# Kernel tuning notes

Hardware: AMD Instinct MI355X
Metric: run time of the kernel (lower is better)

The kernel has to match this reference:

```python
import jax, jax.numpy as jnp
import numpy as np

EMB = 1024
HEAD = 64
RANK = 8
LRA_SCL = 2.0
LORA = 1.0


def setup_inputs() -> dict:
    key = jax.random.key(0)
    ks = jax.random.split(key, 12)
    s = 1.0 / np.sqrt(EMB)
    sr = 1.0 / np.sqrt(RANK)
    inp = {
        "batEmb": jax.random.normal(ks[0], (8, 2048, EMB), dtype=jnp.float32),
        "tokMrk": jax.random.randint(ks[1], (8, 2048), 0, 2, dtype=jnp.int32),
        # base projections, nn.Linear weight layout [out, in]
        "Wq": jax.random.uniform(ks[2], (HEAD, EMB), jnp.float32, -s, s),
        "Wk": jax.random.uniform(ks[3], (HEAD, EMB), jnp.float32, -s, s),
        "Wv": jax.random.uniform(ks[4], (HEAD, EMB), jnp.float32, -s, s),
        # LoRA: A [rank, emb], B [head, rank]. (Original inits B to zero; we
        # randomize with small scale so the LoRA path is numerically exercised.)
        "Aq": jax.random.uniform(ks[5], (RANK, EMB), jnp.float32, -s, s),
        "Bq": jax.random.uniform(ks[6], (HEAD, RANK), jnp.float32, -sr, sr) * 0.02,
        "Ak": jax.random.uniform(ks[7], (RANK, EMB), jnp.float32, -s, s),
        "Bk": jax.random.uniform(ks[8], (HEAD, RANK), jnp.float32, -sr, sr) * 0.02,
        "Av": jax.random.uniform(ks[9], (RANK, EMB), jnp.float32, -s, s),
        "Bv": jax.random.uniform(ks[10], (HEAD, RANK), jnp.float32, -sr, sr) * 0.02,
    }
    return inp


def _proj(x, W, A, B):
    # base + LoRA low-rank delta (dropout = identity in eval)
    base = jnp.einsum('bse,he->bsh', x, W)
    lora = jnp.einsum('bsr,hr->bsh', jnp.einsum('bse,re->bsr', x, A), B)
    return base + lora * (LRA_SCL * LORA)


def reference(batEmb, tokMrk, Wq, Wk, Wv, Aq, Bq, Ak, Bk, Av, Bv):
    q = _proj(batEmb, Wq, Aq, Bq)  # [B,S,H]
    k = _proj(batEmb, Wk, Ak, Bk)
    v = _proj(batEmb, Wv, Av, Bv)
    w = jnp.einsum('bqh,bkh->bqk', q, k) * (HEAD ** -0.5)  # [B,S,S]
    mask = (tokMrk == 0)[:, None, :]  # [B,1,S] over key dim
    w = jnp.where(mask, -jnp.inf, w)
    w = jax.nn.softmax(w, axis=-1)
    w = jnp.nan_to_num(w, nan=0.0)
    return jnp.einsum('bqk,bkh->bqh', w, v)
```

## Files before the change

### kernel.cpp

```cpp
#include <hip/hip_runtime.h>
#include <hip/hip_bf16.h>
#include <stdint.h>

#define EMB 1024
#define NB 8
#define SEQ 2048
#define RANK 8
#define SPLIT 4

#define BM 64
#define BK 64
#define NSTG 16
#define BUFB 40960
#define NBUF 3

typedef __attribute__((ext_vector_type(8))) short bf16x8;
typedef __attribute__((ext_vector_type(4))) float f32x4;
typedef unsigned short u16;
typedef unsigned int u32;

__device__ __forceinline__ u16 f2bf(float f) {
  u32 u = __builtin_bit_cast(u32, f);
  u = (u + 0x7fffu + ((u >> 16) & 1u)) >> 16;
  return (u16)u;
}
__device__ __forceinline__ u32 pk2(float lo, float hi) {
  return (u32)f2bf(lo) | ((u32)f2bf(hi) << 16);
}
__device__ __forceinline__ u32 cvtpk(float lo, float hi) {
  __hip_bfloat162 h = __float22bfloat162_rn(make_float2(lo, hi));
  u32 u; __builtin_memcpy(&u, &h, 4); return u;
}
__device__ __forceinline__ void gll16(const void* g, void* l) {
  __builtin_amdgcn_global_load_lds(
      (const __attribute__((address_space(1))) unsigned int*)g,
      (__attribute__((address_space(3))) unsigned int*)l, 16, 0, 0);
}

#define PBAR()   asm volatile("s_barrier" ::: "memory")
#define WAITV(n) asm volatile("s_waitcnt vmcnt(" #n ")" ::: "memory")

__global__ __launch_bounds__(256) void fold_k(
    const float* __restrict__ Wq, const float* __restrict__ Wk, const float* __restrict__ Wv,
    const float* __restrict__ Aq, const float* __restrict__ Bq,
    const float* __restrict__ Ak, const float* __restrict__ Bk,
    const float* __restrict__ Av, const float* __restrict__ Bv,
    u16* __restrict__ weff) {
  int m = blockIdx.x;
  int mat = m >> 6, h = m & 63;
  const float* W = mat == 0 ? Wq : (mat == 1 ? Wk : Wv);
  const float* A = mat == 0 ? Aq : (mat == 1 ? Ak : Av);
  const float* B = mat == 0 ? Bq : (mat == 1 ? Bk : Bv);
  float bb[RANK];
#pragma unroll
  for (int r = 0; r < RANK; r++) bb[r] = 2.0f * B[h * RANK + r];
  int e = threadIdx.x * 4;
  float4 w4 = *(const float4*)(W + h * EMB + e);
  float a0 = w4.x, a1 = w4.y, a2 = w4.z, a3 = w4.w;
#pragma unroll
  for (int r = 0; r < RANK; r++) {
    float4 av = *(const float4*)(A + r * EMB + e);
    a0 += bb[r] * av.x; a1 += bb[r] * av.y; a2 += bb[r] * av.z; a3 += bb[r] * av.w;
  }
  u16* o = weff + (size_t)m * EMB + e;
  o[0] = f2bf(a0); o[1] = f2bf(a1); o[2] = f2bf(a2); o[3] = f2bf(a3);
}

__global__ __launch_bounds__(320) void proj_k(
    const float* __restrict__ X, const u16* __restrict__ weff,
    u16* __restrict__ qws, u16* __restrict__ kws, u16* __restrict__ vws) {
  extern __shared__ __align__(16) char smem[];

  int t = threadIdx.x;
  int w = t >> 6, l = t & 63;
  int rbase = blockIdx.x * BM;

  if (w >= 3) {
    int q = w - 3;
    int wkoff = ((l & 7) ^ (l >> 3)) * 8;
    int wc0 = l >> 3;
    int lr4 = l >> 4;
    int l15 = l & 15;

#define ISSUE(st, bufp) do {                                                   \
    _Pragma("unroll")                                                          \
    for (int i_ = 0; i_ < 8; i_++) {                                           \
      int rrel_ = q * 32 + i_ * 4 + lr4;                                       \
      int xo_ = 4 * (l15 ^ (rrel_ & 7));        \
      gll16(X + (size_t)(rbase + rrel_) * EMB + (st) * BK + xo_,               \
            (bufp) + q * 8192 + i_ * 1024);                                    \
    }                                                                          \
    _Pragma("unroll")                                                          \
    for (int i_ = 0; i_ < 12; i_++) { int wj_ = q * 12 + i_;                   \
      gll16(weff + (size_t)(wj_ * 8 + wc0) * EMB + (st) * BK + wkoff,          \
            (bufp) + 16384 + wj_ * 1024);                                      \
    } } while (0)

    ISSUE(0, smem);
    ISSUE(1, smem + BUFB);
    WAITV(20);
    for (int s = 0; s < NSTG; s++) {
      PBAR();
      if (s + 2 < NSTG) {
        ISSUE(s + 2, smem + ((s + 2) % NBUF) * BUFB);
        WAITV(20);
      } else if (s + 1 < NSTG) {
        WAITV(0);
      }
    }
#undef ISSUE
  } else {
    int l15 = l & 15, lh = l >> 4;
    f32x4 acc[4][4];
    f32x4 zero = {0.f, 0.f, 0.f, 0.f};
#pragma unroll
    for (int rt = 0; rt < 4; rt++)
#pragma unroll
      for (int ct = 0; ct < 4; ct++) acc[rt][ct] = zero;

    for (int s = 0; s < NSTG; s++) {
      PBAR();
      const char* bx = smem + (s % NBUF) * BUFB;
      const char* bw = bx + 16384;
#pragma unroll
      for (int j = 0; j < 2; j++) {
        bf16x8 a[4];
#pragma unroll
        for (int rt = 0; rt < 4; rt++) {
          int r = rt * 16 + l15;
          int sw = (r & 7) << 4;
          const char* base = bx + r * 256;
          f32x4 lo = *(const f32x4*)(base + ((j * 128 + lh * 32) ^ sw));
          f32x4 hi = *(const f32x4*)(base + ((j * 128 + lh * 32 + 16) ^ sw));
          union { bf16x8 v; u32 u[4]; } au;
          au.u[0] = cvtpk(lo.x, lo.y); au.u[1] = cvtpk(lo.z, lo.w);
          au.u[2] = cvtpk(hi.x, hi.y); au.u[3] = cvtpk(hi.z, hi.w);
          a[rt] = au.v;
        }
        __builtin_amdgcn_s_setprio(1);
#pragma unroll
        for (int ct = 0; ct < 4; ct++) {
          int col = w * 64 + ct * 16 + l15;
          bf16x8 bf = *(const bf16x8*)(bw + col * 128 +
                                       ((j * 64 + lh * 16) ^ ((col & 7) << 4)));
#pragma unroll
          for (int rt = 0; rt < 4; rt++)
            acc[rt][ct] = __builtin_amdgcn_mfma_f32_16x16x32_bf16(a[rt], bf, acc[rt][ct], 0, 0, 0);
        }
        __builtin_amdgcn_s_setprio(0);
      }
    }

#pragma unroll
    for (int rt = 0; rt < 4; rt++)
#pragma unroll
      for (int ct = 0; ct < 4; ct++) {
        int c = w * 64 + ct * 16 + l15;
#pragma unroll
        for (int r = 0; r < 4; r++) {
          int rr = rbase + rt * 16 + lh * 4 + r;
          float av = acc[rt][ct][r];
          if (c < 64) av *= 0.125f;
          u16 v = f2bf(av);
          if (c < 64) {
            qws[(size_t)rr * 64 + c] = v;
          } else if (c < 128) {
            kws[(size_t)rr * 64 + (c - 64)] = v;
          } else {
            int bb = rr >> 11, tok = rr & 2047;
            vws[((size_t)(bb * 64 + (c - 128))) * SEQ + tok] = v;
          }
        }
      }
  }
}

__global__ __launch_bounds__(256) void attn_k(
    const u16* __restrict__ qws, const u16* __restrict__ kws, const u16* __restrict__ vws,
    const int* __restrict__ mrk,
    float* __restrict__ po, float* __restrict__ pmp, float* __restrict__ plp) {
  __shared__ __align__(16) u16 ks[2 * 4096];
  __shared__ __align__(16) u16 vt[2 * 4096];
  __shared__ __align__(16) u16 ps[4 * 1024];

  int b = blockIdx.y;
  int z = blockIdx.z;
  int q0 = blockIdx.x * 64;
  int t = threadIdx.x;
  int w = t >> 6, l = t & 63;
  int l15 = l & 15, lh = l >> 4;

  int srow = t >> 3;
  int ssw = (((t & 7) << 4) ^ ((srow & 7) << 4)) >> 1;
  char* ksb = (char*)ks + w * 1024;
  char* vtb = (char*)vt + w * 1024;

  const u16* qp = qws + ((size_t)(b * SEQ + q0 + w * 16 + l15)) * 64 + lh * 8;
  bf16x8 qb0 = *(const bf16x8*)qp;
  bf16x8 qb1 = *(const bf16x8*)(qp + 32);

  f32x4 o[4];
  f32x4 zero = {0.f, 0.f, 0.f, 0.f};
#pragma unroll
  for (int ht = 0; ht < 4; ht++) o[ht] = zero;
  float mrow = -30000.0f, lrow = 0.f;

  int swz = (l15 & 7) << 4;
  int koffA = ((lh << 4) ^ swz) >> 1;
  int koffB = ((64 | (lh << 4)) ^ swz) >> 1;
  u16* psw = ps + w * 1024 + l15 * 64;

  const int NC = SEQ / 64 / SPLIT;
  int kk0 = z * (SEQ / SPLIT);

#define STAGE_KV(buf, kk)                                                          \
  do {                                                                             \
    gll16(kws + ((size_t)(b * SEQ + (kk) + srow)) * 64 + ssw,                      \
          ksb + (buf) * 8192);                                                     \
    gll16(kws + ((size_t)(b * SEQ + (kk) + srow + 32)) * 64 + ssw,                 \
          ksb + (buf) * 8192 + 4096);                                              \
    gll16(vws + ((size_t)(b * 64 + srow)) * SEQ + (kk) + ssw,                      \
          vtb + (buf) * 8192);                                                     \
    gll16(vws + ((size_t)(b * 64 + srow + 32)) * SEQ + (kk) + ssw,                 \
          vtb + (buf) * 8192 + 4096);                                              \
  } while (0)

  STAGE_KV(0, kk0);
  __syncthreads();

  int cur = 0;
  for (int kc = 0; kc < NC; kc++) {
    int kk = kk0 + kc * 64;
    if (kc + 1 < NC) STAGE_KV(cur ^ 1, kk + 64);

    int4 mi[4];
#pragma unroll
    for (int nt = 0; nt < 4; nt++)
      mi[nt] = *(const int4*)(mrk + b * SEQ + kk + nt * 16 + lh * 4);

    const u16* kb = ks + cur * 4096;
    f32x4 sa[4];
    __builtin_amdgcn_s_setprio(1);
#pragma unroll
    for (int nt = 0; nt < 4; nt++) {
      const u16* kr = kb + (nt * 16 + l15) * 64;
      bf16x8 k0 = *(const bf16x8*)(kr + koffA);
      bf16x8 k1 = *(const bf16x8*)(kr + koffB);
      f32x4 s = zero;
      s = __builtin_amdgcn_mfma_f32_16x16x32_bf16(k0, qb0, s, 0, 0, 0);
      s = __builtin_amdgcn_mfma_f32_16x16x32_bf16(k1, qb1, s, 0, 0, 0);
      sa[nt] = s;
    }
    __builtin_amdgcn_s_setprio(0);

    const u16* vbb = vt + cur * 4096;
    bf16x8 vb[4][2];
#pragma unroll
    for (int ht = 0; ht < 4; ht++) {
      const u16* vr = vbb + (ht * 16 + l15) * 64;
      vb[ht][0] = *(const bf16x8*)(vr + koffA);
      vb[ht][1] = *(const bf16x8*)(vr + koffB);
    }

#pragma unroll
    for (int nt = 0; nt < 4; nt++) {
      sa[nt][0] = mi[nt].x ? sa[nt][0] : -INFINITY;
      sa[nt][1] = mi[nt].y ? sa[nt][1] : -INFINITY;
      sa[nt][2] = mi[nt].z ? sa[nt][2] : -INFINITY;
      sa[nt][3] = mi[nt].w ? sa[nt][3] : -INFINITY;
    }
    float t0 = fmaxf(fmaxf(sa[0][0], sa[0][1]), fmaxf(sa[0][2], sa[0][3]));
    float t1 = fmaxf(fmaxf(sa[1][0], sa[1][1]), fmaxf(sa[1][2], sa[1][3]));
    float t2 = fmaxf(fmaxf(sa[2][0], sa[2][1]), fmaxf(sa[2][2], sa[2][3]));
    float t3 = fmaxf(fmaxf(sa[3][0], sa[3][1]), fmaxf(sa[3][2], sa[3][3]));
    float tm = fmaxf(fmaxf(t0, t1), fmaxf(t2, t3));
    tm = fmaxf(tm, __shfl_xor(tm, 16));
    tm = fmaxf(tm, __shfl_xor(tm, 32));

    if (!__all(tm <= mrow + 8.0f)) {
      float nm = fmaxf(mrow, tm);
      float alpha = __expf(mrow - nm);
      mrow = nm;
      lrow *= alpha;
      float a0 = __shfl(alpha, lh * 4 + 0);
      float a1 = __shfl(alpha, lh * 4 + 1);
      float a2 = __shfl(alpha, lh * 4 + 2);
      float a3 = __shfl(alpha, lh * 4 + 3);
#pragma unroll
      for (int ht = 0; ht < 4; ht++) {
        o[ht][0] *= a0; o[ht][1] *= a1; o[ht][2] *= a2; o[ht][3] *= a3;
      }
    }

    float ts = 0.f;
#pragma unroll
    for (int nt = 0; nt < 4; nt++) {
#pragma unroll
      for (int r = 0; r < 4; r++) {
        float p = __expf(sa[nt][r] - mrow);
        sa[nt][r] = p;
        ts += p;
      }
    }
    ts += __shfl_xor(ts, 16);
    ts += __shfl_xor(ts, 32);
    lrow += ts;

#pragma unroll
    for (int nt = 0; nt < 4; nt++) {
      u32 plo = pk2(sa[nt][0], sa[nt][1]);
      u32 phi = pk2(sa[nt][2], sa[nt][3]);
      *(uint2*)&psw[(((nt * 32 + lh * 8) ^ swz) >> 1)] = make_uint2(plo, phi);
    }
    bf16x8 ap0 = *(const bf16x8*)(psw + koffA);
    bf16x8 ap1 = *(const bf16x8*)(psw + koffB);

    __builtin_amdgcn_s_setprio(1);
#pragma unroll
    for (int ht = 0; ht < 4; ht++) {
      o[ht] = __builtin_amdgcn_mfma_f32_16x16x32_bf16(ap0, vb[ht][0], o[ht], 0, 0, 0);
      o[ht] = __builtin_amdgcn_mfma_f32_16x16x32_bf16(ap1, vb[ht][1], o[ht], 0, 0, 0);
    }
    __builtin_amdgcn_s_setprio(0);
    __syncthreads();
    cur ^= 1;
  }
#undef STAGE_KV

#pragma unroll
  for (int r = 0; r < 4; r++) {
    int rr = q0 + w * 16 + lh * 4 + r;
    float* pob = po + ((size_t)z * NB * SEQ + (size_t)b * SEQ + rr) * 64;
#pragma unroll
    for (int ht = 0; ht < 4; ht++) pob[ht * 16 + l15] = o[ht][r];
  }
  if (lh == 0) {
    int rr = q0 + w * 16 + l15;
    pmp[(size_t)z * NB * SEQ + (size_t)b * SEQ + rr] = mrow;
    plp[(size_t)z * NB * SEQ + (size_t)b * SEQ + rr] = lrow;
  }
}

__global__ __launch_bounds__(256) void merge_k(
    const float* __restrict__ po, const float* __restrict__ pmp,
    const float* __restrict__ plp, float* __restrict__ out) {
  int tid = threadIdx.x;
  int row = blockIdx.x * 32 + (tid >> 3);
  int c8 = (tid & 7) * 8;
  const int RT = NB * SEQ;

  float m[SPLIT], lv[SPLIT];
  float M = -INFINITY;
#pragma unroll
  for (int s = 0; s < SPLIT; s++) {
    m[s] = pmp[(size_t)s * RT + row];
    lv[s] = plp[(size_t)s * RT + row];
    M = fmaxf(M, m[s]);
  }
  float o8[8];
#pragma unroll
  for (int j = 0; j < 8; j++) o8[j] = 0.f;
  float L = 0.f;
  if (M != -INFINITY) {
#pragma unroll
    for (int s = 0; s < SPLIT; s++) {
      float ws = __expf(m[s] - M);
      L += ws * lv[s];
      const float* p = po + ((size_t)s * RT + row) * 64 + c8;
#pragma unroll
      for (int j = 0; j < 8; j++) o8[j] += ws * p[j];
    }
  }
  float inv = (L > 0.f) ? 1.0f / L : 0.f;
  float* op = out + (size_t)row * 64 + c8;
#pragma unroll
  for (int j = 0; j < 8; j++) op[j] = o8[j] * inv;
}

extern "C" void kernel_launch(void* const* d_in, const int* in_sizes, int n_in,
                              void* d_out, int out_size, void* d_ws, size_t ws_size,
                              hipStream_t stream) {
  const float* X   = (const float*)d_in[0];
  const int*   mrk = (const int*)d_in[1];
  const float* Wq  = (const float*)d_in[2];
  const float* Wk  = (const float*)d_in[3];
  const float* Wv  = (const float*)d_in[4];
  const float* Aq  = (const float*)d_in[5];
  const float* Bq  = (const float*)d_in[6];
  const float* Ak  = (const float*)d_in[7];
  const float* Bk  = (const float*)d_in[8];
  const float* Av  = (const float*)d_in[9];
  const float* Bv  = (const float*)d_in[10];

  u16* weff = (u16*)d_ws;
  u16* qws  = (u16*)((char*)d_ws + (512 << 10));
  u16* kws  = qws + (size_t)16384 * 64;
  u16* vws  = kws + (size_t)16384 * 64;
  float* po  = (float*)((char*)d_ws + ((size_t)6656 << 10));
  float* pmp = po + (size_t)SPLIT * 16384 * 64;
  float* plp = pmp + (size_t)SPLIT * 16384;

  (void)hipFuncSetAttribute((const void*)proj_k,
                            hipFuncAttributeMaxDynamicSharedMemorySize, NBUF * BUFB);

  fold_k<<<192, 256, 0, stream>>>(Wq, Wk, Wv, Aq, Bq, Ak, Bk, Av, Bv, weff);
  proj_k<<<256, 320, NBUF * BUFB, stream>>>(X, weff, qws, kws, vws);
  attn_k<<<dim3(32, 8, SPLIT), 256, 0, stream>>>(qws, kws, vws, mrk, po, pmp, plp);
  merge_k<<<512, 256, 0, stream>>>(po, pmp, plp, (float*)d_out);
}
```

Before: 61.64 us.

## Load projection weights directly into registers and halve proj row tile

```diff
diff --git a/kernel.cpp b/kernel.cpp
--- a/kernel.cpp
+++ b/kernel.cpp
@@ -8,10 +8,10 @@
 #define RANK 8
 #define SPLIT 4
 
-#define BM 64
+#define BM 32
 #define BK 64
 #define NSTG 16
-#define BUFB 40960
+#define BUFB 8192
 #define NBUF 3
 
 typedef __attribute__((ext_vector_type(8))) short bf16x8;
@@ -77,56 +77,67 @@
 
   if (w >= 3) {
     int q = w - 3;
-    int wkoff = ((l & 7) ^ (l >> 3)) * 8;
-    int wc0 = l >> 3;
     int lr4 = l >> 4;
     int l15 = l & 15;
 
 #define ISSUE(st, bufp) do {                                                   \
     _Pragma("unroll")                                                          \
-    for (int i_ = 0; i_ < 8; i_++) {                                           \
-      int rrel_ = q * 32 + i_ * 4 + lr4;                                       \
+    for (int i_ = 0; i_ < 4; i_++) {                                           \
+      int rrel_ = q * 16 + i_ * 4 + lr4;                                       \
       int xo_ = 4 * (l15 ^ (rrel_ & 7));        \
       gll16(X + (size_t)(rbase + rrel_) * EMB + (st) * BK + xo_,               \
-            (bufp) + q * 8192 + i_ * 1024);                                    \
-    }                                                                          \
-    _Pragma("unroll")                                                          \
-    for (int i_ = 0; i_ < 12; i_++) { int wj_ = q * 12 + i_;                   \
-      gll16(weff + (size_t)(wj_ * 8 + wc0) * EMB + (st) * BK + wkoff,          \
-            (bufp) + 16384 + wj_ * 1024);                                      \
+            (bufp) + q * 4096 + i_ * 1024);                                    \
     } } while (0)
 
     ISSUE(0, smem);
     ISSUE(1, smem + BUFB);
-    WAITV(20);
+    WAITV(4);
     for (int s = 0; s < NSTG; s++) {
       PBAR();
       if (s + 2 < NSTG) {
         ISSUE(s + 2, smem + ((s + 2) % NBUF) * BUFB);
-        WAITV(20);
-      } else if (s + 1 < NSTG) {
+        WAITV(4);
+      } else {
         WAITV(0);
       }
     }
 #undef ISSUE
   } else {
     int l15 = l & 15, lh = l >> 4;
-    f32x4 acc[4][4];
+    f32x4 acc[2][4];
     f32x4 zero = {0.f, 0.f, 0.f, 0.f};
 #pragma unroll
-    for (int rt = 0; rt < 4; rt++)
+    for (int rt = 0; rt < 2; rt++)
 #pragma unroll
       for (int ct = 0; ct < 4; ct++) acc[rt][ct] = zero;
+
+    const u16* wp[4];
+#pragma unroll
+    for (int ct = 0; ct < 4; ct++)
+      wp[ct] = weff + (size_t)(w * 64 + ct * 16 + l15) * EMB + lh * 8;
+
+    bf16x8 wc[2][4], wn[2][4];
+#pragma unroll
+    for (int j = 0; j < 2; j++)
+#pragma unroll
+      for (int ct = 0; ct < 4; ct++)
+        wc[j][ct] = *(const bf16x8*)(wp[ct] + j * 32);
 
     for (int s = 0; s < NSTG; s++) {
       PBAR();
+      if (s + 1 < NSTG) {
+#pragma unroll
+        for (int j = 0; j < 2; j++)
+#pragma unroll
+          for (int ct = 0; ct < 4; ct++)
+            wn[j][ct] = *(const bf16x8*)(wp[ct] + (s + 1) * BK + j * 32);
+      }
       const char* bx = smem + (s % NBUF) * BUFB;
-      const char* bw = bx + 16384;
 #pragma unroll
       for (int j = 0; j < 2; j++) {
-        bf16x8 a[4];
-#pragma unroll
-        for (int rt = 0; rt < 4; rt++) {
+        bf16x8 a[2];
+#pragma unroll
+        for (int rt = 0; rt < 2; rt++) {
           int r = rt * 16 + l15;
           int sw = (r & 7) << 4;
           const char* base = bx + r * 256;
@@ -139,20 +150,20 @@
         }
         __builtin_amdgcn_s_setprio(1);
 #pragma unroll
-        for (int ct = 0; ct < 4; ct++) {
-          int col = w * 64 + ct * 16 + l15;
-          bf16x8 bf = *(const bf16x8*)(bw + col * 128 +
-                                       ((j * 64 + lh * 16) ^ ((col & 7) << 4)));
-#pragma unroll
-          for (int rt = 0; rt < 4; rt++)
-            acc[rt][ct] = __builtin_amdgcn_mfma_f32_16x16x32_bf16(a[rt], bf, acc[rt][ct], 0, 0, 0);
-        }
+        for (int ct = 0; ct < 4; ct++)
+#pragma unroll
+          for (int rt = 0; rt < 2; rt++)
+            acc[rt][ct] = __builtin_amdgcn_mfma_f32_16x16x32_bf16(a[rt], wc[j][ct], acc[rt][ct], 0, 0, 0);
         __builtin_amdgcn_s_setprio(0);
       }
-    }
-
-#pragma unroll
-    for (int rt = 0; rt < 4; rt++)
+#pragma unroll
+      for (int j = 0; j < 2; j++)
+#pragma unroll
+        for (int ct = 0; ct < 4; ct++) wc[j][ct] = wn[j][ct];
+    }
+
+#pragma unroll
+    for (int rt = 0; rt < 2; rt++)
 #pragma unroll
       for (int ct = 0; ct < 4; ct++) {
         int c = w * 64 + ct * 16 + l15;
@@ -404,7 +415,7 @@
                             hipFuncAttributeMaxDynamicSharedMemorySize, NBUF * BUFB);
 
   fold_k<<<192, 256, 0, stream>>>(Wq, Wk, Wv, Aq, Bq, Ak, Bk, Av, Bv, weff);
-  proj_k<<<256, 320, NBUF * BUFB, stream>>>(X, weff, qws, kws, vws);
+  proj_k<<<512, 320, NBUF * BUFB, stream>>>(X, weff, qws, kws, vws);
   attn_k<<<dim3(32, 8, SPLIT), 256, 0, stream>>>(qws, kws, vws, mrk, po, pmp, plp);
   merge_k<<<512, 256, 0, stream>>>(po, pmp, plp, (float*)d_out);
 }
```

Result: slower. 70.23 us (+13.9%).

## Halve projection row tile and split X/W buffers to launch more blocks

Applied to the files above, without the earlier changes.

```diff
diff --git a/kernel.cpp b/kernel.cpp
--- a/kernel.cpp
+++ b/kernel.cpp
@@ -8,11 +8,11 @@
 #define RANK 8
 #define SPLIT 4
 
-#define BM 64
+#define BM 32
 #define BK 64
 #define NSTG 16
-#define BUFB 40960
-#define NBUF 3
+#define XBUF 8192
+#define WBUF 24576
 
 typedef __attribute__((ext_vector_type(8))) short bf16x8;
 typedef __attribute__((ext_vector_type(4))) float f32x4;
@@ -70,6 +70,8 @@
     const float* __restrict__ X, const u16* __restrict__ weff,
     u16* __restrict__ qws, u16* __restrict__ kws, u16* __restrict__ vws) {
   extern __shared__ __align__(16) char smem[];
+  char* xsm = smem;
+  char* wsm = smem + 3 * XBUF;
 
   int t = threadIdx.x;
   int w = t >> 6, l = t & 63;
@@ -77,56 +79,69 @@
 
   if (w >= 3) {
     int q = w - 3;
-    int wkoff = ((l & 7) ^ (l >> 3)) * 8;
-    int wc0 = l >> 3;
     int lr4 = l >> 4;
     int l15 = l & 15;
-
-#define ISSUE(st, bufp) do {                                                   \
+    int wc0 = l >> 3;
+    int wkoff = ((l & 7) ^ wc0) * 8;
+
+#define ISSX(st, bufp) do {                                                    \
     _Pragma("unroll")                                                          \
-    for (int i_ = 0; i_ < 8; i_++) {                                           \
-      int rrel_ = q * 32 + i_ * 4 + lr4;                                       \
+    for (int i_ = 0; i_ < 2; i_++) {                                           \
+      int rrel_ = q * 16 + i_ * 8 + lr4 * 2 + (l15 >> 3);                      \
+      int sl_ = l15 & 7;                                 \
+      (void)sl_;                                                               \
+    } } while (0)
+#undef ISSX
+
+#define ISSUE_X(st, bufp) do {                                                 \
+    _Pragma("unroll")                                                          \
+    for (int i_ = 0; i_ < 4; i_++) {                                           \
+      int rrel_ = q * 16 + i_ * 4 + lr4;                                       \
       int xo_ = 4 * (l15 ^ (rrel_ & 7));        \
       gll16(X + (size_t)(rbase + rrel_) * EMB + (st) * BK + xo_,               \
-            (bufp) + q * 8192 + i_ * 1024);                                    \
-    }                                                                          \
+            (bufp) + q * 4096 + i_ * 1024);                                    \
+    } } while (0)
+
+#define ISSUE_W(st, bufp) do {                                                 \
     _Pragma("unroll")                                                          \
     for (int i_ = 0; i_ < 12; i_++) { int wj_ = q * 12 + i_;                   \
       gll16(weff + (size_t)(wj_ * 8 + wc0) * EMB + (st) * BK + wkoff,          \
-            (bufp) + 16384 + wj_ * 1024);                                      \
+            (bufp) + wj_ * 1024);                                              \
     } } while (0)
 
-    ISSUE(0, smem);
-    ISSUE(1, smem + BUFB);
-    WAITV(20);
+    ISSUE_W(0, wsm);
+    ISSUE_X(0, xsm);
+    ISSUE_X(1, xsm + XBUF);
+    WAITV(4);
+    PBAR();
+    for (int s = 0; s < NSTG; s++) {
+      if (s + 1 < NSTG) ISSUE_W(s + 1, wsm + ((s + 1) & 1) * WBUF);
+      if (s + 2 < NSTG) ISSUE_X(s + 2, xsm + ((s + 2) % 3) * XBUF);
+      if (s + 1 < NSTG) {
+        if (s + 2 < NSTG) { WAITV(4); } else { WAITV(0); }
+        PBAR();
+      }
+    }
+#undef ISSUE_X
+#undef ISSUE_W
+  } else {
+    int l15 = l & 15, lh = l >> 4;
+    f32x4 acc[2][4];
+    f32x4 zero = {0.f, 0.f, 0.f, 0.f};
+#pragma unroll
+    for (int rt = 0; rt < 2; rt++)
+#pragma unroll
+      for (int ct = 0; ct < 4; ct++) acc[rt][ct] = zero;
+
     for (int s = 0; s < NSTG; s++) {
       PBAR();
-      if (s + 2 < NSTG) {
-        ISSUE(s + 2, smem + ((s + 2) % NBUF) * BUFB);
-        WAITV(20);
-      } else if (s + 1 < NSTG) {
-        WAITV(0);
-      }
-    }
-#undef ISSUE
-  } else {
-    int l15 = l & 15, lh = l >> 4;
-    f32x4 acc[4][4];
-    f32x4 zero = {0.f, 0.f, 0.f, 0.f};
-#pragma unroll
-    for (int rt = 0; rt < 4; rt++)
-#pragma unroll
-      for (int ct = 0; ct < 4; ct++) acc[rt][ct] = zero;
-
-    for (int s = 0; s < NSTG; s++) {
-      PBAR();
-      const char* bx = smem + (s % NBUF) * BUFB;
-      const char* bw = bx + 16384;
+      const char* bx = xsm + (s % 3) * XBUF;
+      const char* bw = wsm + (s & 1) * WBUF;
 #pragma unroll
       for (int j = 0; j < 2; j++) {
-        bf16x8 a[4];
-#pragma unroll
-        for (int rt = 0; rt < 4; rt++) {
+        bf16x8 a[2];
+#pragma unroll
+        for (int rt = 0; rt < 2; rt++) {
           int r = rt * 16 + l15;
           int sw = (r & 7) << 4;
           const char* base = bx + r * 256;
@@ -144,7 +159,7 @@
           bf16x8 bf = *(const bf16x8*)(bw + col * 128 +
                                        ((j * 64 + lh * 16) ^ ((col & 7) << 4)));
 #pragma unroll
-          for (int rt = 0; rt < 4; rt++)
+          for (int rt = 0; rt < 2; rt++)
             acc[rt][ct] = __builtin_amdgcn_mfma_f32_16x16x32_bf16(a[rt], bf, acc[rt][ct], 0, 0, 0);
         }
         __builtin_amdgcn_s_setprio(0);
@@ -152,7 +167,7 @@
     }
 
 #pragma unroll
-    for (int rt = 0; rt < 4; rt++)
+    for (int rt = 0; rt < 2; rt++)
 #pragma unroll
       for (int ct = 0; ct < 4; ct++) {
         int c = w * 64 + ct * 16 + l15;
@@ -401,10 +416,11 @@
   float* plp = pmp + (size_t)SPLIT * 16384;
 
   (void)hipFuncSetAttribute((const void*)proj_k,
-                            hipFuncAttributeMaxDynamicSharedMemorySize, NBUF * BUFB);
+                            hipFuncAttributeMaxDynamicSharedMemorySize,
+                            3 * XBUF + 2 * WBUF);
 
   fold_k<<<192, 256, 0, stream>>>(Wq, Wk, Wv, Aq, Bq, Ak, Bk, Av, Bv, weff);
-  proj_k<<<256, 320, NBUF * BUFB, stream>>>(X, weff, qws, kws, vws);
+  proj_k<<<512, 320, 3 * XBUF + 2 * WBUF, stream>>>(X, weff, qws, kws, vws);
   attn_k<<<dim3(32, 8, SPLIT), 256, 0, stream>>>(qws, kws, vws, mrk, po, pmp, plp);
   merge_k<<<512, 256, 0, stream>>>(po, pmp, plp, (float*)d_out);
 }
```

Result: faster. 59.08 us (-4.2%).
